# Performance work log

Hardware: AMD Instinct MI355X
Metric: run time of the kernel (lower is better)

The kernel has to match this reference:

```python
import jax, jax.numpy as jnp
import numpy as np
from itertools import combinations

K = 10          # knn size hardcoded in GFM
SHARP = 20.0    # GMCCE_Sharp
THRESH = 0.5    # GMCCE_Thres
EPS = 1e-6

B, D_EMB, N = 4, 512, 2048


def _pairwise_dist(x):  # x: [B,N,3] -> [B,N,N]
    sq = jnp.sum(x * x, -1)
    d2 = sq[:, :, None] + sq[:, None, :] - 2.0 * jnp.einsum('bnd,bmd->bnm', x, x)
    return jnp.sqrt(jnp.maximum(d2, 0.0))


def _areas(pcd, tri):  # pcd: [B,N,3], tri: [B,N,P,3] int -> [B,N,P] triangle areas
    b = jnp.arange(pcd.shape[0])[:, None, None, None]
    p = pcd[b, tri]                      # [B,N,P,3,3]
    e1 = p[..., 1, :] - p[..., 0, :]
    e2 = p[..., 2, :] - p[..., 0, :]
    return 0.5 * jnp.linalg.norm(jnp.cross(e1, e2), axis=-1)


def _gfm(src, tgt):  # src: [B,3,N], tgt: [B,N,3] -> binary weights [B,N]
    b, _, n = src.shape
    x = src.transpose(0, 2, 1)           # [B,N,3]
    d = _pairwise_dist(x)
    w = jnp.exp(-d * d / 2.0)            # sigma=1
    idx = jax.lax.top_k(w, K)[1]         # [B,N,K] knn indices
    pairs = np.array(list(combinations(range(K), 2)))  # [45,2]
    idx_pairs = idx[:, :, pairs]         # [B,N,45,2]
    anchor = jnp.broadcast_to(jnp.arange(n)[None, :, None, None], (b, n, pairs.shape[0], 1))
    tri = jnp.concatenate([anchor, idx_pairs], axis=-1)  # [B,N,45,3]
    a_s = _areas(x, tri)
    a_t = _areas(tgt, tri)
    z = jnp.zeros_like(a_s)
    # getTri puts area in slot 0 then sorts ascending -> [0,0,area] (area>=0)
    ls = jnp.stack([z, z, a_s], -1)
    lt = jnp.stack([z, z, a_t], -1) + EPS
    loss = jnp.sum((ls - lt) ** 2, -1) / jnp.sum((ls + lt) ** 2, -1)
    loss = jnp.sort(loss, axis=-1)
    reg = jnp.linalg.norm(ls - lt, axis=-1)   # unsorted, as in original
    loss = loss + 0.1 * reg
    med = jnp.median(loss, axis=-1, keepdims=True)
    loss = jnp.where(loss > 3.0 * med, 0.0, loss)
    loss = loss[:, :, :K]
    loss = jnp.mean(jnp.sqrt(loss + EPS), axis=-1)          # [B,N]
    loss = loss - jnp.min(loss, axis=-1, keepdims=True)
    weight = 2.0 * jax.nn.sigmoid(-SHARP * loss)
    return jnp.where(weight > THRESH, 1.0, 0.0)


def _procrustes(X, Y, w):  # X,Y: [N,3], w: [N] -> (R [3,3], t [3])
    eps = 1e-7
    W1 = jnp.sum(jnp.abs(w))
    wn = (w / (W1 + eps))[:, None]
    mux = jnp.sum(wn * X, 0, keepdims=True)
    muy = jnp.sum(wn * Y, 0, keepdims=True)
    Sxy = (Y - muy).T @ (wn * (X - mux))    # 3x3
    U, _, Vh = jnp.linalg.svd(Sxy)
    s = jnp.sign(jnp.linalg.det(U) * jnp.linalg.det(Vh))
    d3 = jnp.stack([jnp.ones(()), jnp.ones(()), s])
    R = (U * d3[None, :]) @ Vh
    t = muy[0] - R @ mux[0]
    return R, t


def setup_inputs() -> dict:
    key = jax.random.key(0)
    k1, k2, k3, k4, k5 = jax.random.split(key, 5)
    return {
        'src_embedding': jax.random.normal(k1, (B, D_EMB, N), jnp.float32),
        'tgt_embedding': jax.random.normal(k2, (B, D_EMB, N), jnp.float32),
        'src': jax.random.normal(k3, (B, 3, N), jnp.float32),
        'tgt': jax.random.normal(k4, (B, 3, N), jnp.float32),
        'temperature': jax.random.uniform(k5, (B,), jnp.float32),
        'is_corr': 1,
    }


def reference(src_embedding, tgt_embedding, src, tgt, temperature, is_corr):
    # corres_mode == True and is_corr == True branch
    d_k = src_embedding.shape[1]
    scores = jnp.einsum('bdn,bdm->bnm', src_embedding, tgt_embedding) / jnp.sqrt(jnp.float32(d_k))
    scores = jax.nn.softmax(10000.0 * scores, axis=2)
    corres = jnp.argmax(scores, axis=-1)                         # [B,N]
    corr_tgt = jnp.einsum('bnm,bmd->bnd', scores, tgt.transpose(0, 2, 1))
    weight = _gfm(src, corr_tgt)                                 # [B,N]
    src_t = src.transpose(0, 2, 1)
    tgt_t = tgt.transpose(0, 2, 1)
    src_corr = jnp.take_along_axis(tgt_t, corres[:, :, None], axis=1)  # [B,N,3]
    w = jax.lax.stop_gradient(weight)                            # weight.detach()
    R, T = jax.vmap(_procrustes)(src_t, src_corr, w)
    return R, T, corres[:, :, None], weight[:, :, None]
```

## Files before the change

### kernel.cpp

```cpp
#include <hip/hip_runtime.h>
#include <hip/hip_bf16.h>

#define NN 2048
#define DD 512
#define NBATCH 4
#define KNB 10
#define NPAIR 45

typedef __attribute__((ext_vector_type(8))) _Float16 f16x8;
typedef __attribute__((ext_vector_type(4))) float f32x4;

__device__ __forceinline__ float tri_area(float p0x, float p0y, float p0z,
                                          float p1x, float p1y, float p1z,
                                          float p2x, float p2y, float p2z) {
    float e1x = __fsub_rn(p1x, p0x), e1y = __fsub_rn(p1y, p0y), e1z = __fsub_rn(p1z, p0z);
    float e2x = __fsub_rn(p2x, p0x), e2y = __fsub_rn(p2y, p0y), e2z = __fsub_rn(p2z, p0z);
    float c0 = __fsub_rn(__fmul_rn(e1y, e2z), __fmul_rn(e1z, e2y));
    float c1 = __fsub_rn(__fmul_rn(e1z, e2x), __fmul_rn(e1x, e2z));
    float c2 = __fsub_rn(__fmul_rn(e1x, e2y), __fmul_rn(e1y, e2x));
    float ss = __fadd_rn(__fadd_rn(__fmul_rn(c0, c0), __fmul_rn(c1, c1)), __fmul_rn(c2, c2));
    return __fmul_rn(0.5f, sqrtf(ss));
}

__device__ __forceinline__ double wave_red_sum_d(double v) {
#pragma unroll
    for (int st = 1; st < 64; st <<= 1) v += __shfl_xor(v, st, 64);
    return v;
}

__global__ __launch_bounds__(256) void prep_planes(const float* __restrict__ srcE,
                                                   const float* __restrict__ tgtE,
                                                   short* __restrict__ Ah,
                                                   short* __restrict__ Bh,
                                                   int* __restrict__ count) {
    int kt = blockIdx.x & 15, ng = blockIdx.x >> 4;
    int b = blockIdx.y, mat = blockIdx.z;
    int t = threadIdx.x;
    if (blockIdx.x == 0 && b == 0 && mat == 0 && t == 0) count[0] = 0;
    int gg = t & 3, nloc = t >> 2;
    int n = ng * 64 + nloc;
    int d0 = kt * 32 + gg * 8;
    const float* src = (mat ? tgtE : srcE) + (size_t)b * DD * NN;
    short* PH = mat ? Bh : Ah;

    float x[8];
#pragma unroll
    for (int j = 0; j < 8; j++) x[j] = src[(size_t)(d0 + j) * NN + n];
    unsigned h4[4];
#pragma unroll
    for (int p = 0; p < 4; p++) {
        _Float16 h0 = (_Float16)x[2 * p], h1 = (_Float16)x[2 * p + 1];
        h4[p] = (unsigned)__builtin_bit_cast(unsigned short, h0) |
                ((unsigned)__builtin_bit_cast(unsigned short, h1) << 16);
    }
    size_t o = ((size_t)(b * 16 + kt) * NN + n) * 32 + ((gg ^ ((n >> 1) & 3)) << 3);
    *(uint4*)&PH[o] = (uint4){h4[0], h4[1], h4[2], h4[3]};
}

__global__ __launch_bounds__(256) void gemm_fused(const short* __restrict__ Ah,
                                                  const short* __restrict__ Bh,
                                                  float* __restrict__ part) {
    int b = blockIdx.z;
    int id = blockIdx.y * 16 + blockIdx.x;
    int swz = (id & 7) * 32 + (id >> 3);
    int bx = swz & 15, by = swz >> 4;
    int n0 = by * 128, m0 = bx * 128;

    __shared__ short LDS[2][2][4096];

    int t = threadIdx.x, w = t >> 6, lane = t & 63;
    int wr = w >> 1, wc = w & 1;
    int fr = lane & 15, kq = lane >> 4;

    const short* gpl[2] = {Ah, Bh};

    f32x4 acc[4][4];
#pragma unroll
    for (int i = 0; i < 4; i++)
#pragma unroll
        for (int j = 0; j < 4; j++) acc[i][j] = (f32x4){0.f, 0.f, 0.f, 0.f};

    auto STAGE = [&](int buf, int kt) {
#pragma unroll
        for (int q = 0; q < 4; q++) {
            int p = q >> 1, h = q & 1;
            int rb = (p == 0) ? n0 : m0;
            const short* g = gpl[p] + ((size_t)(b * 16 + kt) * NN + rb) * 32 +
                             h * 2048 + w * 512 + lane * 8;
            __builtin_amdgcn_global_load_lds(
                (const __attribute__((address_space(1))) void*)g,
                (__attribute__((address_space(3))) void*)&LDS[buf][p][h * 2048 + w * 512],
                16, 0, 0);
        }
    };

    STAGE(0, 0);
    __syncthreads();
    int cur = 0;
    for (int kt = 0; kt < 16; kt++) {
        if (kt < 15) STAGE(cur ^ 1, kt + 1);

        f16x8 ah[4], bh[4];
#pragma unroll
        for (int i = 0; i < 4; i++) {
            int rA = wr * 64 + i * 16 + fr;
            int offA = rA * 32 + ((kq ^ ((rA >> 1) & 3)) << 3);
            ah[i] = *(const f16x8*)&LDS[cur][0][offA];
            int rB = wc * 64 + i * 16 + fr;
            int offB = rB * 32 + ((kq ^ ((rB >> 1) & 3)) << 3);
            bh[i] = *(const f16x8*)&LDS[cur][1][offB];
        }
#pragma unroll
        for (int i = 0; i < 4; i++)
#pragma unroll
            for (int j = 0; j < 4; j++)
                acc[i][j] = __builtin_amdgcn_mfma_f32_16x16x32_f16(ah[i], bh[j],
                                                                   acc[i][j], 0, 0, 0);
        __syncthreads();
        cur ^= 1;
    }

    int t32 = bx * 2 + wc;
#pragma unroll
    for (int i = 0; i < 4; i++) {
#pragma unroll
        for (int rg = 0; rg < 4; rg++) {
            int row = n0 + wr * 64 + i * 16 + kq * 4 + rg;
            float m1 = -3.4e38f, m2 = -3.4e38f;
            int i1 = 0x7fffffff;
#pragma unroll
            for (int j = 0; j < 4; j++) {
                float vv = __fmul_rn(10000.0f, __fdiv_rn(acc[i][j][rg], 22.627416997969522f));
                int col = m0 + wc * 64 + j * 16 + fr;
                if (vv > m1) { m2 = m1; m1 = vv; i1 = col; }
                else if (vv > m2) m2 = vv;
            }
#pragma unroll
            for (int st = 1; st < 16; st <<= 1) {
                float om1 = __shfl_xor(m1, st, 64);
                float om2 = __shfl_xor(m2, st, 64);
                int oi1 = __shfl_xor(i1, st, 64);
                if (om1 > m1 || (om1 == m1 && oi1 < i1)) {
                    m2 = fmaxf(m1, om2); m1 = om1; i1 = oi1;
                } else {
                    m2 = fmaxf(om1, m2);
                }
            }
            if (fr == 0) {
                size_t o = ((size_t)(b * NN + row) * 32 + t32) * 4;
                *(float4*)&part[o] = (float4){m1, m2, (float)i1, 0.f};
            }
        }
    }
}

__global__ __launch_bounds__(256) void combine_rows(const float* __restrict__ part,
                                                    const float* __restrict__ tgtP,
                                                    int* __restrict__ corres,
                                                    int* __restrict__ flags,
                                                    int* __restrict__ list,
                                                    int* __restrict__ count,
                                                    unsigned long long* __restrict__ keys,
                                                    float* __restrict__ corrTgt) {
    int b = blockIdx.y;
    int w = threadIdx.x >> 6, lane = threadIdx.x & 63;
    int n = blockIdx.x * 4 + w;
    int row = b * NN + n;
    float m1 = -3.4e38f, m2 = -3.4e38f;
    int i1 = 0x7fffffff;
    if (lane < 32) {
        float4 p1 = *(const float4*)&part[((size_t)row * 32 + lane) * 4];
        m1 = p1.x; m2 = p1.y; i1 = (int)p1.z;
    }
    float tm1 = m1;
#pragma unroll
    for (int st = 1; st < 64; st <<= 1) {
        float om1 = __shfl_xor(m1, st, 64);
        float om2 = __shfl_xor(m2, st, 64);
        int oi1 = __shfl_xor(i1, st, 64);
        if (om1 > m1 || (om1 == m1 && oi1 < i1)) {
            m2 = fmaxf(m1, om2); m1 = om1; i1 = oi1;
        } else {
            m2 = fmaxf(om1, m2);
        }
    }
    int fl = (__fsub_rn(m1, m2) < 34.0f) ? 1 : 0;
    bool pred = fl && (lane < 32) && (tm1 >= __fsub_rn(m1, 44.0f));
    unsigned long long mask = __ballot(pred);
    int base = 0;
    if (fl) {
        if (lane == 0) {
            flags[row] = 1;
            keys[row] = 0ull;
            base = atomicAdd(count, __popcll(mask));
        }
        base = __shfl(base, 0, 64);
        if (pred) {
            int rank = __popcll(mask & ((1ull << lane) - 1ull));
            list[base + rank] = (row << 5) | lane;
        }
    } else if (lane == 0) {
        flags[row] = 0;
    }
    if (lane == 0) {
        corres[row] = i1;
        const float* tb = tgtP + (size_t)b * 3 * NN;
        corrTgt[(size_t)row * 3 + 0] = tb[i1];
        corrTgt[(size_t)row * 3 + 1] = tb[NN + i1];
        corrTgt[(size_t)row * 3 + 2] = tb[2 * NN + i1];
    }
}

__global__ __launch_bounds__(256) void refine_tiles(const float* __restrict__ A,
                                                    const float* __restrict__ Bm,
                                                    const int* __restrict__ list,
                                                    const int* __restrict__ count,
                                                    unsigned long long* __restrict__ keys) {
    int tid = threadIdx.x;
    int c = tid & 63, ks = tid >> 6;
    __shared__ float Acol[DD];
    __shared__ float partial[4][64];
    int nitems = count[0];
    for (int item = blockIdx.x; item < nitems; item += 2048) {
        int code = list[item];
        int row = code >> 5, tile = code & 31;
        int b = row / NN, n = row % NN;
        const float* Ab = A + (size_t)b * DD * NN;
        const float* Bb = Bm + (size_t)b * DD * NN;
        Acol[tid] = Ab[(size_t)tid * NN + n];
        Acol[tid + 256] = Ab[(size_t)(tid + 256) * NN + n];
        __syncthreads();
        int m = tile * 64 + c;
        float acc = 0.f;
        int dbase = ks * 128;
        for (int d = 0; d < 128; d++)
            acc = fmaf(Acol[dbase + d], Bb[(size_t)(dbase + d) * NN + m], acc);
        partial[ks][c] = acc;
        __syncthreads();
        if (tid < 64) {
            float tot = __fadd_rn(__fadd_rn(partial[0][c], partial[1][c]),
                                  __fadd_rn(partial[2][c], partial[3][c]));
            float sc = __fmul_rn(10000.0f, __fdiv_rn(tot, 22.627416997969522f));
            unsigned u = __float_as_uint(sc);
            u = (u & 0x80000000u) ? ~u : (u | 0x80000000u);
            unsigned long long key =
                ((unsigned long long)u << 32) | (unsigned)(~(unsigned)m);
#pragma unroll
            for (int st = 1; st < 64; st <<= 1) {
                unsigned long long ok = __shfl_xor((long long)key, st, 64);
                if (ok > key) key = ok;
            }
            if (c == 0) atomicMax(&keys[row], key);
        }
        __syncthreads();
    }
}

__global__ __launch_bounds__(512) void gfm_kernel(const float* __restrict__ srcP,
                                                  const float* __restrict__ corrTgt,
                                                  float* __restrict__ pointLoss) {
    int b = blockIdx.y, tid = threadIdx.x;
    int w = tid >> 6, lane = tid & 63;
    int n = blockIdx.x * 8 + w;
    __shared__ float4 XP[NN];
    __shared__ int nbl[8][KNB];
    __shared__ float ptb[8][KNB][3];
    __shared__ float la[8][NPAIR], rg[8][NPAIR], srt[8][NPAIR];
    const float* xs = srcP + (size_t)b * 3 * NN;

    for (int i = tid; i < NN / 4; i += 512) {
        float4 u0 = ((const float4*)xs)[i];
        float4 u1 = ((const float4*)(xs + NN))[i];
        float4 u2 = ((const float4*)(xs + 2 * NN))[i];
        float4 q;
        q.x = __fadd_rn(__fadd_rn(__fmul_rn(u0.x, u0.x), __fmul_rn(u1.x, u1.x)), __fmul_rn(u2.x, u2.x));
        q.y = __fadd_rn(__fadd_rn(__fmul_rn(u0.y, u0.y), __fmul_rn(u1.y, u1.y)), __fmul_rn(u2.y, u2.y));
        q.z = __fadd_rn(__fadd_rn(__fmul_rn(u0.z, u0.z), __fmul_rn(u1.z, u1.z)), __fmul_rn(u2.z, u2.z));
        q.w = __fadd_rn(__fadd_rn(__fmul_rn(u0.w, u0.w), __fmul_rn(u1.w, u1.w)), __fmul_rn(u2.w, u2.w));
        XP[4 * i + 0] = (float4){u0.x, u1.x, u2.x, q.x};
        XP[4 * i + 1] = (float4){u0.y, u1.y, u2.y, q.y};
        XP[4 * i + 2] = (float4){u0.z, u1.z, u2.z, q.z};
        XP[4 * i + 3] = (float4){u0.w, u1.w, u2.w, q.w};
    }
    __syncthreads();

    float4 av = XP[n];
    float a0 = av.x, a1 = av.y, a2 = av.z, sqa = av.w;
    unsigned key[32];
#pragma unroll
    for (int r = 0; r < 32; r++) {
        int m = lane + 64 * r;
        float4 p = XP[m];
        float dot = __fadd_rn(__fadd_rn(__fmul_rn(a0, p.x), __fmul_rn(a1, p.y)),
                              __fmul_rn(a2, p.z));
        float d2 = __fsub_rn(__fadd_rn(sqa, p.w), __fmul_rn(2.0f, dot));
        d2 = fmaxf(d2, 0.0f);
        key[r] = (__float_as_uint(d2) & 0xFFFFF800u) | (unsigned)m;
    }
    unsigned removed = 0;
#pragma unroll
    for (int it = 0; it < KNB; it++) {
        unsigned best = 0xFFFFFFFFu;
#pragma unroll
        for (int r = 0; r < 32; r++) {
            unsigned kk = ((removed >> r) & 1u) ? 0xFFFFFFFFu : key[r];
            best = min(best, kk);
        }
#pragma unroll
        for (int st = 1; st < 64; st <<= 1) {
            unsigned ob = __shfl_xor((int)best, st, 64);
            best = min(best, ob);
        }
        int m = (int)(best & 2047u);
        if (lane == 0) nbl[w][it] = m;
        removed |= ((m & 63) == lane) ? (1u << (m >> 6)) : 0u;
    }
    __builtin_amdgcn_wave_barrier();
    if (lane < KNB) {
        int ia = nbl[w][lane];
        const float* ct = corrTgt + ((size_t)b * NN + ia) * 3;
        ptb[w][lane][0] = ct[0];
        ptb[w][lane][1] = ct[1];
        ptb[w][lane][2] = ct[2];
    }
    __builtin_amdgcn_wave_barrier();
    const float* ctn = corrTgt + ((size_t)b * NN + n) * 3;
    float t0 = ctn[0], t1 = ctn[1], t2 = ctn[2];
    if (lane < NPAIR) {
        int k = lane, ja = 0, cnt = 9;
        while (k >= cnt) { k -= cnt; ja++; cnt--; }
        int jb = ja + 1 + k;
        int ia = nbl[w][ja], ib = nbl[w][jb];
        float4 pa = XP[ia], pb = XP[ib];
        float area_s = tri_area(a0, a1, a2, pa.x, pa.y, pa.z, pb.x, pb.y, pb.z);
        float area_t = tri_area(t0, t1, t2, ptb[w][ja][0], ptb[w][ja][1], ptb[w][ja][2],
                                ptb[w][jb][0], ptb[w][jb][1], ptb[w][jb][2]);
        const float EPSF = 1e-6f;
        float ee = __fmul_rn(EPSF, EPSF);
        float lt2 = __fadd_rn(area_t, EPSF);
        float da = __fsub_rn(area_s, lt2);
        float sa = __fadd_rn(area_s, lt2);
        float num = __fadd_rn(__fadd_rn(ee, ee), __fmul_rn(da, da));
        float den = __fadd_rn(__fadd_rn(ee, ee), __fmul_rn(sa, sa));
        la[w][lane] = __fdiv_rn(num, den);
        rg[w][lane] = sqrtf(num);
    }
    __builtin_amdgcn_wave_barrier();
    if (lane < NPAIR) {
        float x = la[w][lane];
        int rk = 0;
        for (int j = 0; j < NPAIR; j++) {
            float y = la[w][j];
            rk += (y < x || (y == x && j < lane)) ? 1 : 0;
        }
        srt[w][rk] = x;
    }
    __builtin_amdgcn_wave_barrier();
    float l2v = 0.f;
    if (lane < NPAIR) l2v = __fadd_rn(srt[w][lane], __fmul_rn(0.1f, rg[w][lane]));
    __builtin_amdgcn_wave_barrier();
    if (lane < NPAIR) la[w][lane] = l2v;
    __builtin_amdgcn_wave_barrier();
    if (lane < NPAIR) {
        float x = la[w][lane];
        int rk = 0;
        for (int j = 0; j < NPAIR; j++) {
            float y = la[w][j];
            rk += (y < x || (y == x && j < lane)) ? 1 : 0;
        }
        srt[w][rk] = x;
    }
    __builtin_amdgcn_wave_barrier();
    float med = srt[w][22];
    float thr = __fmul_rn(3.0f, med);
    float term = 0.f;
    if (lane < KNB) {
        float vv = la[w][lane];
        if (vv > thr) vv = 0.f;
        term = sqrtf(__fadd_rn(vv, 1e-6f));
    }
#pragma unroll
    for (int st = 1; st < 64; st <<= 1) term += __shfl_xor(term, st, 64);
    if (lane == 0) pointLoss[b * NN + n] = __fdiv_rn(term, 10.0f);
}

__device__ double det3(const double M[3][3]) {
    return M[0][0] * (M[1][1] * M[2][2] - M[1][2] * M[2][1]) -
           M[0][1] * (M[1][0] * M[2][2] - M[1][2] * M[2][0]) +
           M[0][2] * (M[1][0] * M[2][1] - M[1][1] * M[2][0]);
}

__global__ __launch_bounds__(1024) void fused_finish(const float* __restrict__ pointLoss,
                                                     const int* __restrict__ flags,
                                                     const unsigned long long* __restrict__ keys,
                                                     const int* __restrict__ corresIn,
                                                     const float* __restrict__ srcP,
                                                     const float* __restrict__ tgtP,
                                                     float* __restrict__ outR,
                                                     float* __restrict__ outT,
                                                     float* __restrict__ outC,
                                                     float* __restrict__ outW) {
    int b = blockIdx.x, tid = threadIdx.x;
    int w = tid >> 6, lane = tid & 63;
    __shared__ int csh[NN];
    __shared__ float wsh[NN];
    __shared__ float fred[1024];
    __shared__ double sd[16][9];
    __shared__ double sxySh[9];

    float mn = 3.4e38f;
    for (int n = tid; n < NN; n += 1024) {
        int row = b * NN + n;
        int ci = corresIn[row];
        if (flags[row]) ci = (int)(~(unsigned)(keys[row] & 0xFFFFFFFFull));
        csh[n] = ci;
        outC[row] = (float)ci;
        mn = fminf(mn, pointLoss[row]);
    }
    fred[tid] = mn;
    __syncthreads();
    for (int st = 512; st > 0; st >>= 1) {
        if (tid < st) fred[tid] = fminf(fred[tid], fred[tid + st]);
        __syncthreads();
    }
    float minL = fred[0];
    __syncthreads();

    for (int n = tid; n < NN; n += 1024) {
        int row = b * NN + n;
        float l = __fsub_rn(pointLoss[row], minL);
        float z = __fmul_rn(-20.0f, l);
        float ez = expf(z);
        float sg = __fdiv_rn(ez, __fadd_rn(1.0f, ez));
        float wf = (__fmul_rn(2.0f, sg) > 0.5f) ? 1.0f : 0.0f;
        wsh[n] = wf;
        outW[row] = wf;
    }
    __syncthreads();

    const float* xs = srcP + (size_t)b * 3 * NN;
    const float* ts = tgtP + (size_t)b * 3 * NN;
    double acc7[7] = {0, 0, 0, 0, 0, 0, 0};
    for (int n = tid; n < NN; n += 1024) {
        if (wsh[n] != 0.0f) {
            acc7[0] += 1.0;
            acc7[1] += (double)xs[n];
            acc7[2] += (double)xs[NN + n];
            acc7[3] += (double)xs[2 * NN + n];
            int m = csh[n];
            acc7[4] += (double)ts[m];
            acc7[5] += (double)ts[NN + m];
            acc7[6] += (double)ts[2 * NN + m];
        }
    }
#pragma unroll
    for (int q = 0; q < 7; q++) {
        double r = wave_red_sum_d(acc7[q]);
        if (lane == 0) sd[w][q] = r;
    }
    __syncthreads();
    double tot7[7];
#pragma unroll
    for (int q = 0; q < 7; q++) {
        double s2 = 0;
#pragma unroll
        for (int w2 = 0; w2 < 16; w2++) s2 += sd[w2][q];
        tot7[q] = s2;
    }
    __syncthreads();

    double W1e = tot7[0] + 1e-7;
    double mux0 = tot7[1] / W1e, mux1 = tot7[2] / W1e, mux2 = tot7[3] / W1e;
    double muy0 = tot7[4] / W1e, muy1 = tot7[5] / W1e, muy2 = tot7[6] / W1e;

    double s[9] = {0, 0, 0, 0, 0, 0, 0, 0, 0};
    for (int n = tid; n < NN; n += 1024) {
        if (wsh[n] != 0.0f) {
            double dx0 = (double)xs[n] - mux0;
            double dx1 = (double)xs[NN + n] - mux1;
            double dx2 = (double)xs[2 * NN + n] - mux2;
            int m = csh[n];
            double dy0 = (double)ts[m] - muy0;
            double dy1 = (double)ts[NN + m] - muy1;
            double dy2 = (double)ts[2 * NN + m] - muy2;
            s[0] += dy0 * dx0; s[1] += dy0 * dx1; s[2] += dy0 * dx2;
            s[3] += dy1 * dx0; s[4] += dy1 * dx1; s[5] += dy1 * dx2;
            s[6] += dy2 * dx0; s[7] += dy2 * dx1; s[8] += dy2 * dx2;
        }
    }
#pragma unroll
    for (int q = 0; q < 9; q++) {
        double r = wave_red_sum_d(s[q]);
        if (lane == 0) sd[w][q] = r;
    }
    __syncthreads();
    if (tid < 9) {
        double s2 = 0;
#pragma unroll
        for (int w2 = 0; w2 < 16; w2++) s2 += sd[w2][tid];
        sxySh[tid] = s2 / W1e;
    }
    __syncthreads();

    if (tid == 0) {
        double Bm2[3][3], V[3][3];
        for (int r = 0; r < 3; r++)
            for (int c2 = 0; c2 < 3; c2++) {
                Bm2[r][c2] = sxySh[r * 3 + c2];
                V[r][c2] = (r == c2) ? 1.0 : 0.0;
            }
        double nrm2 = 0;
        for (int r = 0; r < 3; r++)
            for (int c2 = 0; c2 < 3; c2++) nrm2 += Bm2[r][c2] * Bm2[r][c2];

        for (int sweep = 0; sweep < 60; sweep++) {
            double off = 0;
            for (int p = 0; p < 2; p++) {
                for (int q = p + 1; q < 3; q++) {
                    double al = 0, be = 0, ga = 0;
                    for (int i = 0; i < 3; i++) {
                        al += Bm2[i][p] * Bm2[i][p];
                        be += Bm2[i][q] * Bm2[i][q];
                        ga += Bm2[i][p] * Bm2[i][q];
                    }
                    off += ga * ga;
                    if (fabs(ga) > 1e-300) {
                        double ze = (be - al) / (2.0 * ga);
                        double tt = copysign(1.0, ze) / (fabs(ze) + sqrt(1.0 + ze * ze));
                        double c = 1.0 / sqrt(1.0 + tt * tt), sn = c * tt;
                        for (int i = 0; i < 3; i++) {
                            double bp = Bm2[i][p], bq = Bm2[i][q];
                            Bm2[i][p] = c * bp - sn * bq;
                            Bm2[i][q] = sn * bp + c * bq;
                            double vp = V[i][p], vq = V[i][q];
                            V[i][p] = c * vp - sn * vq;
                            V[i][q] = sn * vp + c * vq;
                        }
                    }
                }
            }
            if (off <= 1e-30 * nrm2 * nrm2) break;
        }
        double sig[3];
        for (int j = 0; j < 3; j++) {
            double ss = 0;
            for (int i = 0; i < 3; i++) ss += Bm2[i][j] * Bm2[i][j];
            sig[j] = sqrt(ss);
        }
        for (int a = 0; a < 2; a++)
            for (int j = 0; j < 2 - a; j++)
                if (sig[j] < sig[j + 1]) {
                    double t2 = sig[j]; sig[j] = sig[j + 1]; sig[j + 1] = t2;
                    for (int i = 0; i < 3; i++) {
                        double tb = Bm2[i][j]; Bm2[i][j] = Bm2[i][j + 1]; Bm2[i][j + 1] = tb;
                        double tv = V[i][j]; V[i][j] = V[i][j + 1]; V[i][j + 1] = tv;
                    }
                }
        double U[3][3];
        for (int j = 0; j < 3; j++) {
            double inv = (sig[j] > 1e-150) ? 1.0 / sig[j] : 0.0;
            for (int i = 0; i < 3; i++) U[i][j] = Bm2[i][j] * inv;
        }
        if (sig[2] <= 1e-10 * (sig[0] + 1e-300)) {
            double u0 = U[1][0] * U[2][1] - U[2][0] * U[1][1];
            double u1 = U[2][0] * U[0][1] - U[0][0] * U[2][1];
            double u2 = U[0][0] * U[1][1] - U[1][0] * U[0][1];
            double nr = sqrt(u0 * u0 + u1 * u1 + u2 * u2);
            if (nr > 1e-150) { U[0][2] = u0 / nr; U[1][2] = u1 / nr; U[2][2] = u2 / nr; }
        }
        double dU = det3(U), dV = det3(V);
        double s3 = (dU * dV >= 0.0) ? 1.0 : -1.0;
        double R[3][3];
        for (int i = 0; i < 3; i++)
            for (int j = 0; j < 3; j++)
                R[i][j] = U[i][0] * V[j][0] + U[i][1] * V[j][1] + s3 * U[i][2] * V[j][2];
        double mux[3] = {mux0, mux1, mux2};
        double muy[3] = {muy0, muy1, muy2};
        for (int i = 0; i < 3; i++) {
            for (int j = 0; j < 3; j++) outR[b * 9 + i * 3 + j] = (float)R[i][j];
            double t2 = muy[i] - (R[i][0] * mux[0] + R[i][1] * mux[1] + R[i][2] * mux[2]);
            outT[b * 3 + i] = (float)t2;
        }
    }
}

extern "C" void kernel_launch(void* const* d_in, const int* in_sizes, int n_in,
                              void* d_out, int out_size, void* d_ws, size_t ws_size,
                              hipStream_t stream) {
    const float* srcE = (const float*)d_in[0];
    const float* tgtE = (const float*)d_in[1];
    const float* srcP = (const float*)d_in[2];
    const float* tgtP = (const float*)d_in[3];
    float* out = (float*)d_out;

    char* w = (char*)d_ws;
    size_t off = 0;
    auto alloc = [&](size_t bytes) -> void* {
        void* p = w + off;
        off = (off + bytes + 255) & ~(size_t)255;
        return p;
    };
    float* corrTgt = (float*)alloc((size_t)NBATCH * NN * 3 * 4);
    int* corres = (int*)alloc((size_t)NBATCH * NN * 4);
    int* flags = (int*)alloc((size_t)NBATCH * NN * 4);
    unsigned long long* keys = (unsigned long long*)alloc((size_t)NBATCH * NN * 8);
    int* list = (int*)alloc((size_t)NBATCH * NN * 32 * 4);
    int* count = (int*)alloc(256);
    float* pointLoss = (float*)alloc((size_t)NBATCH * NN * 4);
    size_t planeShorts = (size_t)NBATCH * 16 * NN * 32;
    short* Ah = (short*)alloc(planeShorts * 2);
    short* Bh = (short*)alloc(planeShorts * 2);
    float* part = (float*)alloc((size_t)NBATCH * NN * 32 * 4 * 4);

    prep_planes<<<dim3(512, NBATCH, 2), 256, 0, stream>>>(srcE, tgtE, Ah, Bh, count);
    gemm_fused<<<dim3(NN / 128, NN / 128, NBATCH), 256, 0, stream>>>(Ah, Bh, part);
    combine_rows<<<dim3(NN / 4, NBATCH), 256, 0, stream>>>(part, tgtP, corres, flags, list,
                                                           count, keys, corrTgt);
    gfm_kernel<<<dim3(NN / 8, NBATCH), 512, 0, stream>>>(srcP, corrTgt, pointLoss);
    refine_tiles<<<dim3(2048), 256, 0, stream>>>(srcE, tgtE, list, count, keys);
    fused_finish<<<NBATCH, 1024, 0, stream>>>(pointLoss, flags, keys, corres, srcP, tgtP,
                                              out, out + 36, out + 48, out + 48 + NBATCH * NN);
}
```

Before: 128.8 us.

## Process two query points per wave in GFM kernel and remap prep_planes threads

The GFM kernel now has each wave handle two query points. It computes distance keys for both against each loaded point, so every shared-memory point read serves two rows, and the grid is halved. This cuts the per-block cost of staging the full point cloud into LDS and the number of XP reads. In exchange it doubles the key registers per thread (64), which may lower occupancy or cause spills. Separately, prep_planes swaps the thread-to-(n, d-group) mapping so consecutive threads read consecutive n, giving coalesced global loads, though the swizzled 16-byte stores become more scattered.

```diff
diff --git a/kernel.cpp b/kernel.cpp
--- a/kernel.cpp
+++ b/kernel.cpp
@@ -37,7 +37,7 @@
     int b = blockIdx.y, mat = blockIdx.z;
     int t = threadIdx.x;
     if (blockIdx.x == 0 && b == 0 && mat == 0 && t == 0) count[0] = 0;
-    int gg = t & 3, nloc = t >> 2;
+    int nloc = t & 63, gg = t >> 6;
     int n = ng * 64 + nloc;
     int d0 = kt * 32 + gg * 8;
     const float* src = (mat ? tgtE : srcE) + (size_t)b * DD * NN;
@@ -261,11 +261,11 @@
                                                   float* __restrict__ pointLoss) {
     int b = blockIdx.y, tid = threadIdx.x;
     int w = tid >> 6, lane = tid & 63;
-    int n = blockIdx.x * 8 + w;
+    int nbase = blockIdx.x * 16 + w * 2;
     __shared__ float4 XP[NN];
-    __shared__ int nbl[8][KNB];
-    __shared__ float ptb[8][KNB][3];
-    __shared__ float la[8][NPAIR], rg[8][NPAIR], srt[8][NPAIR];
+    __shared__ int nbl[16][KNB];
+    __shared__ float ptb[16][KNB][3];
+    __shared__ float la[16][NPAIR], rg[16][NPAIR], srt[16][NPAIR];
     const float* xs = srcP + (size_t)b * 3 * NN;
 
     for (int i = tid; i < NN / 4; i += 512) {
@@ -284,104 +284,117 @@
     }
     __syncthreads();
 
-    float4 av = XP[n];
-    float a0 = av.x, a1 = av.y, a2 = av.z, sqa = av.w;
-    unsigned key[32];
+    float4 av[2];
+    av[0] = XP[nbase];
+    av[1] = XP[nbase + 1];
+    unsigned key[2][32];
 #pragma unroll
     for (int r = 0; r < 32; r++) {
         int m = lane + 64 * r;
         float4 p = XP[m];
-        float dot = __fadd_rn(__fadd_rn(__fmul_rn(a0, p.x), __fmul_rn(a1, p.y)),
-                              __fmul_rn(a2, p.z));
-        float d2 = __fsub_rn(__fadd_rn(sqa, p.w), __fmul_rn(2.0f, dot));
-        d2 = fmaxf(d2, 0.0f);
-        key[r] = (__float_as_uint(d2) & 0xFFFFF800u) | (unsigned)m;
-    }
-    unsigned removed = 0;
-#pragma unroll
-    for (int it = 0; it < KNB; it++) {
-        unsigned best = 0xFFFFFFFFu;
-#pragma unroll
-        for (int r = 0; r < 32; r++) {
-            unsigned kk = ((removed >> r) & 1u) ? 0xFFFFFFFFu : key[r];
-            best = min(best, kk);
-        }
-#pragma unroll
-        for (int st = 1; st < 64; st <<= 1) {
-            unsigned ob = __shfl_xor((int)best, st, 64);
-            best = min(best, ob);
-        }
-        int m = (int)(best & 2047u);
-        if (lane == 0) nbl[w][it] = m;
-        removed |= ((m & 63) == lane) ? (1u << (m >> 6)) : 0u;
-    }
-    __builtin_amdgcn_wave_barrier();
-    if (lane < KNB) {
-        int ia = nbl[w][lane];
-        const float* ct = corrTgt + ((size_t)b * NN + ia) * 3;
-        ptb[w][lane][0] = ct[0];
-        ptb[w][lane][1] = ct[1];
-        ptb[w][lane][2] = ct[2];
-    }
-    __builtin_amdgcn_wave_barrier();
-    const float* ctn = corrTgt + ((size_t)b * NN + n) * 3;
-    float t0 = ctn[0], t1 = ctn[1], t2 = ctn[2];
-    if (lane < NPAIR) {
-        int k = lane, ja = 0, cnt = 9;
-        while (k >= cnt) { k -= cnt; ja++; cnt--; }
-        int jb = ja + 1 + k;
-        int ia = nbl[w][ja], ib = nbl[w][jb];
-        float4 pa = XP[ia], pb = XP[ib];
-        float area_s = tri_area(a0, a1, a2, pa.x, pa.y, pa.z, pb.x, pb.y, pb.z);
-        float area_t = tri_area(t0, t1, t2, ptb[w][ja][0], ptb[w][ja][1], ptb[w][ja][2],
-                                ptb[w][jb][0], ptb[w][jb][1], ptb[w][jb][2]);
-        const float EPSF = 1e-6f;
-        float ee = __fmul_rn(EPSF, EPSF);
-        float lt2 = __fadd_rn(area_t, EPSF);
-        float da = __fsub_rn(area_s, lt2);
-        float sa = __fadd_rn(area_s, lt2);
-        float num = __fadd_rn(__fadd_rn(ee, ee), __fmul_rn(da, da));
-        float den = __fadd_rn(__fadd_rn(ee, ee), __fmul_rn(sa, sa));
-        la[w][lane] = __fdiv_rn(num, den);
-        rg[w][lane] = sqrtf(num);
-    }
-    __builtin_amdgcn_wave_barrier();
-    if (lane < NPAIR) {
-        float x = la[w][lane];
-        int rk = 0;
-        for (int j = 0; j < NPAIR; j++) {
-            float y = la[w][j];
-            rk += (y < x || (y == x && j < lane)) ? 1 : 0;
-        }
-        srt[w][rk] = x;
-    }
-    __builtin_amdgcn_wave_barrier();
-    float l2v = 0.f;
-    if (lane < NPAIR) l2v = __fadd_rn(srt[w][lane], __fmul_rn(0.1f, rg[w][lane]));
-    __builtin_amdgcn_wave_barrier();
-    if (lane < NPAIR) la[w][lane] = l2v;
-    __builtin_amdgcn_wave_barrier();
-    if (lane < NPAIR) {
-        float x = la[w][lane];
-        int rk = 0;
-        for (int j = 0; j < NPAIR; j++) {
-            float y = la[w][j];
-            rk += (y < x || (y == x && j < lane)) ? 1 : 0;
-        }
-        srt[w][rk] = x;
-    }
-    __builtin_amdgcn_wave_barrier();
-    float med = srt[w][22];
-    float thr = __fmul_rn(3.0f, med);
-    float term = 0.f;
-    if (lane < KNB) {
-        float vv = la[w][lane];
-        if (vv > thr) vv = 0.f;
-        term = sqrtf(__fadd_rn(vv, 1e-6f));
-    }
-#pragma unroll
-    for (int st = 1; st < 64; st <<= 1) term += __shfl_xor(term, st, 64);
-    if (lane == 0) pointLoss[b * NN + n] = __fdiv_rn(term, 10.0f);
+#pragma unroll
+        for (int pp = 0; pp < 2; pp++) {
+            float dot = __fadd_rn(__fadd_rn(__fmul_rn(av[pp].x, p.x), __fmul_rn(av[pp].y, p.y)),
+                                  __fmul_rn(av[pp].z, p.z));
+            float d2 = __fsub_rn(__fadd_rn(av[pp].w, p.w), __fmul_rn(2.0f, dot));
+            d2 = fmaxf(d2, 0.0f);
+            key[pp][r] = (__float_as_uint(d2) & 0xFFFFF800u) | (unsigned)m;
+        }
+    }
+
+#pragma unroll
+    for (int pp = 0; pp < 2; pp++) {
+        int slot = w * 2 + pp;
+        int n = nbase + pp;
+        float a0 = av[pp].x, a1 = av[pp].y, a2 = av[pp].z;
+
+        unsigned removed = 0;
+#pragma unroll
+        for (int it = 0; it < KNB; it++) {
+            unsigned best = 0xFFFFFFFFu;
+#pragma unroll
+            for (int r = 0; r < 32; r++) {
+                unsigned kk = ((removed >> r) & 1u) ? 0xFFFFFFFFu : key[pp][r];
+                best = min(best, kk);
+            }
+#pragma unroll
+            for (int st = 1; st < 64; st <<= 1) {
+                unsigned ob = __shfl_xor((int)best, st, 64);
+                best = min(best, ob);
+            }
+            int m = (int)(best & 2047u);
+            if (lane == 0) nbl[slot][it] = m;
+            removed |= ((m & 63) == lane) ? (1u << (m >> 6)) : 0u;
+        }
+        __builtin_amdgcn_wave_barrier();
+        if (lane < KNB) {
+            int ia = nbl[slot][lane];
+            const float* ct = corrTgt + ((size_t)b * NN + ia) * 3;
+            ptb[slot][lane][0] = ct[0];
+            ptb[slot][lane][1] = ct[1];
+            ptb[slot][lane][2] = ct[2];
+        }
+        __builtin_amdgcn_wave_barrier();
+        const float* ctn = corrTgt + ((size_t)b * NN + n) * 3;
+        float t0 = ctn[0], t1 = ctn[1], t2 = ctn[2];
+        if (lane < NPAIR) {
+            int k = lane, ja = 0, cnt = 9;
+            while (k >= cnt) { k -= cnt; ja++; cnt--; }
+            int jb = ja + 1 + k;
+            int ia = nbl[slot][ja], ib = nbl[slot][jb];
+            float4 pa = XP[ia], pb = XP[ib];
+            float area_s = tri_area(a0, a1, a2, pa.x, pa.y, pa.z, pb.x, pb.y, pb.z);
+            float area_t = tri_area(t0, t1, t2, ptb[slot][ja][0], ptb[slot][ja][1],
+                                    ptb[slot][ja][2], ptb[slot][jb][0], ptb[slot][jb][1],
+                                    ptb[slot][jb][2]);
+            const float EPSF = 1e-6f;
+            float ee = __fmul_rn(EPSF, EPSF);
+            float lt2 = __fadd_rn(area_t, EPSF);
+            float da = __fsub_rn(area_s, lt2);
+            float sa = __fadd_rn(area_s, lt2);
+            float num = __fadd_rn(__fadd_rn(ee, ee), __fmul_rn(da, da));
+            float den = __fadd_rn(__fadd_rn(ee, ee), __fmul_rn(sa, sa));
+            la[slot][lane] = __fdiv_rn(num, den);
+            rg[slot][lane] = sqrtf(num);
+        }
+        __builtin_amdgcn_wave_barrier();
+        if (lane < NPAIR) {
+            float x = la[slot][lane];
+            int rk = 0;
+            for (int j = 0; j < NPAIR; j++) {
+                float y = la[slot][j];
+                rk += (y < x || (y == x && j < lane)) ? 1 : 0;
+            }
+            srt[slot][rk] = x;
+        }
+        __builtin_amdgcn_wave_barrier();
+        float l2v = 0.f;
+        if (lane < NPAIR) l2v = __fadd_rn(srt[slot][lane], __fmul_rn(0.1f, rg[slot][lane]));
+        __builtin_amdgcn_wave_barrier();
+        if (lane < NPAIR) la[slot][lane] = l2v;
+        __builtin_amdgcn_wave_barrier();
+        if (lane < NPAIR) {
+            float x = la[slot][lane];
+            int rk = 0;
+            for (int j = 0; j < NPAIR; j++) {
+                float y = la[slot][j];
+                rk += (y < x || (y == x && j < lane)) ? 1 : 0;
+            }
+            srt[slot][rk] = x;
+        }
+        __builtin_amdgcn_wave_barrier();
+        float med = srt[slot][22];
+        float thr = __fmul_rn(3.0f, med);
+        float term = 0.f;
+        if (lane < KNB) {
+            float vv = la[slot][lane];
+            if (vv > thr) vv = 0.f;
+            term = sqrtf(__fadd_rn(vv, 1e-6f));
+        }
+#pragma unroll
+        for (int st = 1; st < 64; st <<= 1) term += __shfl_xor(term, st, 64);
+        if (lane == 0) pointLoss[b * NN + n] = __fdiv_rn(term, 10.0f);
+    }
 }
 
 __device__ double det3(const double M[3][3]) {
@@ -616,7 +629,7 @@
     gemm_fused<<<dim3(NN / 128, NN / 128, NBATCH), 256, 0, stream>>>(Ah, Bh, part);
     combine_rows<<<dim3(NN / 4, NBATCH), 256, 0, stream>>>(part, tgtP, corres, flags, list,
                                                            count, keys, corrTgt);
-    gfm_kernel<<<dim3(NN / 8, NBATCH), 512, 0, stream>>>(srcP, corrTgt, pointLoss);
+    gfm_kernel<<<dim3(NN / 16, NBATCH), 512, 0, stream>>>(srcP, corrTgt, pointLoss);
     refine_tiles<<<dim3(2048), 256, 0, stream>>>(srcE, tgtE, list, count, keys);
     fused_finish<<<NBATCH, 1024, 0, stream>>>(pointLoss, flags, keys, corres, srcP, tgtP,
                                               out, out + 36, out + 48, out + 48 + NBATCH * NN);
```

After: 144.7 us. +12.3%, slower.
